# Performance work log

Measured on AMD Instinct MI355X. Metric: run time of the kernel, lower is better.

## Reference

```python
import jax, jax.numpy as jnp
import numpy as np

NEG_SLOPE = 0.2
LN_EPS = 1e-5


def _gat_layer(x, src, dst, W, a_src, a_dst, N):
    # x: [N, Fin], W: [Fin, H*C], a_src/a_dst: [H, C]
    H, C = a_src.shape
    h = (x @ W).reshape(N, H, C)
    al_src = (h * a_src).sum(-1)  # [N, H]
    al_dst = (h * a_dst).sum(-1)  # [N, H]
    e = jax.nn.leaky_relu(al_src[src] + al_dst[dst], NEG_SLOPE)  # [E, H]
    m = jax.ops.segment_max(e, dst, num_segments=N)
    e = jnp.exp(e - m[dst])
    denom = jax.ops.segment_sum(e, dst, num_segments=N)
    alpha = e / denom[dst]  # softmax over incoming edges per dst node
    msg = h[src] * alpha[:, :, None]  # [E, H, C]
    return jax.ops.segment_sum(msg, dst, num_segments=N)  # [N, H, C]


def _layer_norm(x, g, b):
    mu = x.mean(-1, keepdims=True)
    var = ((x - mu) ** 2).mean(-1, keepdims=True)
    return (x - mu) * jax.lax.rsqrt(var + LN_EPS) * g + b


def setup_inputs() -> dict:
    key = jax.random.key(0)
    ks = jax.random.split(key, 20)
    N, E, Fin, Ch, H = 50000, 800000, 128, 64, 4
    s = lambda k, shp, sc=0.05: jax.random.normal(k, shp, dtype=jnp.float32) * sc
    return {
        "x": jax.random.normal(ks[0], (N, Fin), dtype=jnp.float32),
        "edge_index": jax.random.randint(ks[1], (2, E), 0, N, dtype=jnp.int64),
        "W1": s(ks[2], (Fin, H * Ch)),
        "att_src1": s(ks[3], (H, Ch)),
        "att_dst1": s(ks[4], (H, Ch)),
        "b1": jnp.zeros((H * Ch,), jnp.float32),
        "ln1_g": jnp.ones((H * Ch,), jnp.float32),
        "ln1_b": jnp.zeros((H * Ch,), jnp.float32),
        "W2": s(ks[5], (H * Ch, Ch)),
        "att_src2": s(ks[6], (1, Ch)),
        "att_dst2": s(ks[7], (1, Ch)),
        "b2": jnp.zeros((Ch,), jnp.float32),
        "ln2_g": jnp.ones((Ch,), jnp.float32),
        "ln2_b": jnp.zeros((Ch,), jnp.float32),
        "fc1_W": s(ks[8], (Ch, Ch // 2)),
        "fc1_b": jnp.zeros((Ch // 2,), jnp.float32),
        "fc2_W": s(ks[9], (Ch // 2, 1)),
        "fc2_b": jnp.zeros((1,), jnp.float32),
    }


def reference(x, edge_index, W1, att_src1, att_dst1, b1, ln1_g, ln1_b,
              W2, att_src2, att_dst2, b2, ln2_g, ln2_b,
              fc1_W, fc1_b, fc2_W, fc2_b):
    N = x.shape[0]
    # PyG GATConv adds self-loops by default
    loop = jnp.arange(N, dtype=edge_index.dtype)
    src = jnp.concatenate([edge_index[0], loop])
    dst = jnp.concatenate([edge_index[1], loop])

    # GAT layer 1 (heads=4, concat) + LayerNorm + ReLU (dropout is identity in eval)
    h = _gat_layer(x, src, dst, W1, att_src1, att_dst1, N).reshape(N, -1) + b1
    h = jax.nn.relu(_layer_norm(h, ln1_g, ln1_b))

    # GAT layer 2 (heads=1) + LayerNorm + ReLU
    h = _gat_layer(h, src, dst, W2, att_src2, att_dst2, N).reshape(N, -1) + b2
    h = jax.nn.relu(_layer_norm(h, ln2_g, ln2_b))

    # MLP head
    h = jax.nn.relu(h @ fc1_W + fc1_b)
    return h @ fc2_W + fc2_b  # [N, 1]
```

## Files before the change

### kernel.cpp

```cpp
#include <hip/hip_runtime.h>
#include <hip/hip_fp16.h>
#include <math.h>

#define NEG_SLOPE 0.2f
#define LN_EPS 1e-5f
#define SCCHUNK 8192
#define PADCAP 64
#define CURPAD 32

typedef __attribute__((ext_vector_type(8))) _Float16 half8;
typedef __attribute__((ext_vector_type(4))) _Float16 half4;
typedef __attribute__((ext_vector_type(4))) float floatx4;

static __device__ __forceinline__ float lrelu(float e) {
    return e > 0.0f ? e : NEG_SLOPE * e;
}

__global__ __launch_bounds__(256) void k_scatter(
    const int* __restrict__ ei, unsigned* __restrict__ cursor,
    unsigned short* __restrict__ eidx, int N, int E)
{
    const int tid = threadIdx.x;
    const unsigned basev = cursor[(size_t)N * CURPAD];
    const int Et = E + N;
    const int i0 = blockIdx.x * SCCHUNK;

    int s[32], d[32];
    unsigned pos[32];

#pragma unroll
    for (int j = 0; j < 32; ++j) {
        const int i = i0 + j * 256 + tid;
        if (i < Et) {
            if (i < E) { s[j] = ei[i]; d[j] = ei[E + i]; }
            else       { s[j] = d[j] = i - E; }
        } else {
            d[j] = -1;
        }
    }
#pragma unroll
    for (int j = 0; j < 32; ++j) {
        if (d[j] >= 0)
            pos[j] = atomicAdd(&cursor[(size_t)d[j] * CURPAD], 1u);
    }
#pragma unroll
    for (int j = 0; j < 32; ++j) {
        if (d[j] >= 0) {
            unsigned p = pos[j] - basev;
            if (p < PADCAP) eidx[(size_t)d[j] * PADCAP + p] = (unsigned short)s[j];
        }
    }
}

__global__ __launch_bounds__(256) void k_gemm1(
    const float* __restrict__ x, const float* __restrict__ W1,
    const float* __restrict__ as1, const float* __restrict__ ad1,
    _Float16* __restrict__ h1, float* __restrict__ als, float* __restrict__ ald,
    int N)
{
    const int tid = threadIdx.x;
    const int lane = tid & 63, w = tid >> 6;
    const int l15 = lane & 15, quad = lane >> 4;
    const int r_base = blockIdx.x * 64;

    half8 B[4][4];
    float asv[4], adv[4];
#pragma unroll
    for (int nt = 0; nt < 4; ++nt) {
        const int n = w * 64 + nt * 16 + l15;
        asv[nt] = as1[n]; adv[nt] = ad1[n];
#pragma unroll
        for (int ks = 0; ks < 4; ++ks) {
            const int k0 = ks * 32 + quad * 8;
            half8 b;
#pragma unroll
            for (int j = 0; j < 8; ++j) b[j] = (_Float16)W1[(size_t)(k0 + j) * 256 + n];
            B[ks][nt] = b;
        }
    }

#pragma unroll
    for (int rt = 0; rt < 4; ++rt) {
        const int r0 = r_base + rt * 16;
        int m = r0 + l15; if (m >= N) m = N - 1;
        half8 A[4];
#pragma unroll
        for (int ks = 0; ks < 4; ++ks) {
            const int k0 = ks * 32 + quad * 8;
            const float4* xp = (const float4*)(x + (size_t)m * 128 + k0);
            float4 v0 = xp[0], v1 = xp[1];
            half8 a;
            a[0] = (_Float16)v0.x; a[1] = (_Float16)v0.y; a[2] = (_Float16)v0.z; a[3] = (_Float16)v0.w;
            a[4] = (_Float16)v1.x; a[5] = (_Float16)v1.y; a[6] = (_Float16)v1.z; a[7] = (_Float16)v1.w;
            A[ks] = a;
        }
        floatx4 C[4];
#pragma unroll
        for (int nt = 0; nt < 4; ++nt) C[nt] = (floatx4){0.f, 0.f, 0.f, 0.f};
#pragma unroll
        for (int ks = 0; ks < 4; ++ks)
#pragma unroll
            for (int nt = 0; nt < 4; ++nt)
                C[nt] = __builtin_amdgcn_mfma_f32_16x16x32_f16(A[ks], B[ks][nt], C[nt], 0, 0, 0);

#pragma unroll
        for (int reg = 0; reg < 4; ++reg) {
            const int row = r0 + quad * 4 + reg;
            float vs = 0.f, vd = 0.f;
#pragma unroll
            for (int nt = 0; nt < 4; ++nt) {
                float c = C[nt][reg];
                if (row < N) h1[(size_t)row * 256 + w * 64 + nt * 16 + l15] = (_Float16)c;
                vs += c * asv[nt]; vd += c * adv[nt];
            }
#pragma unroll
            for (int o = 1; o < 16; o <<= 1) { vs += __shfl_xor(vs, o); vd += __shfl_xor(vd, o); }
            if (l15 == 0 && row < N) { als[row * 4 + w] = vs; ald[row * 4 + w] = vd; }
        }
    }
}

__global__ __launch_bounds__(256) void k_agg1(
    const _Float16* __restrict__ h1, const float* __restrict__ als, const float* __restrict__ ald,
    const unsigned* __restrict__ cursor, const unsigned short* __restrict__ eidx,
    const float* __restrict__ b1, const float* __restrict__ g1, const float* __restrict__ be1,
    _Float16* __restrict__ hln1, int N)
{
    __shared__ float alp[4][64][4];
    const int wv = threadIdx.x >> 6, lane = threadIdx.x & 63;
    int n = blockIdx.x * 4 + wv;
    if (n >= N) n = N - 1;
    const int base = n * PADCAP;
    const unsigned basev = cursor[(size_t)N * CURPAD];
    int deg = (int)(cursor[(size_t)n * CURPAD] - basev); if (deg > PADCAP) deg = PADCAP;
    const float4 ad = ((const float4*)ald)[n];

    const int srcv = eidx[base + (lane < deg ? lane : deg - 1)];
    float e0 = -1e30f, e1 = -1e30f, e2 = -1e30f, e3 = -1e30f;
    if (lane < deg) {
        float4 a4 = ((const float4*)als)[srcv];
        e0 = lrelu(a4.x + ad.x);
        e1 = lrelu(a4.y + ad.y);
        e2 = lrelu(a4.z + ad.z);
        e3 = lrelu(a4.w + ad.w);
    }
    float m0 = e0, m1 = e1, m2 = e2, m3 = e3;
#pragma unroll
    for (int o = 32; o; o >>= 1) {
        m0 = fmaxf(m0, __shfl_xor(m0, o));
        m1 = fmaxf(m1, __shfl_xor(m1, o));
        m2 = fmaxf(m2, __shfl_xor(m2, o));
        m3 = fmaxf(m3, __shfl_xor(m3, o));
    }
    float p0 = __expf(e0 - m0), p1 = __expf(e1 - m1);
    float p2 = __expf(e2 - m2), p3 = __expf(e3 - m3);
    float s0 = p0, s1 = p1, s2 = p2, s3 = p3;
#pragma unroll
    for (int o = 32; o; o >>= 1) {
        s0 += __shfl_xor(s0, o);
        s1 += __shfl_xor(s1, o);
        s2 += __shfl_xor(s2, o);
        s3 += __shfl_xor(s3, o);
    }
    float4 av;
    av.x = p0 / s0; av.y = p1 / s1; av.z = p2 / s2; av.w = p3 / s3;
    *(float4*)(&alp[wv][lane][0]) = av;

    float4 acc = make_float4(0.f, 0.f, 0.f, 0.f);
    const int hd = lane >> 4;
    const float* alpr = &alp[wv][0][hd];
    const int degr = (deg + 7) & ~7;
    for (int eb = 0; eb < degr; eb += 8) {
#pragma unroll
        for (int u = 0; u < 8; ++u) {
            const int e = eb + u;
            int s = __builtin_amdgcn_readlane(srcv, e);
            float a_e = alpr[e * 4];
            half4 v = *(const half4*)(h1 + (size_t)s * 256 + 4 * lane);
            acc.x = fmaf((float)v.x, a_e, acc.x);
            acc.y = fmaf((float)v.y, a_e, acc.y);
            acc.z = fmaf((float)v.z, a_e, acc.z);
            acc.w = fmaf((float)v.w, a_e, acc.w);
        }
    }

    float4 bb = ((const float4*)b1)[lane];
    float y0 = acc.x + bb.x, y1 = acc.y + bb.y, y2 = acc.z + bb.z, y3 = acc.w + bb.w;
    float ps = y0 + y1 + y2 + y3;
    float pss = y0 * y0 + y1 * y1 + y2 * y2 + y3 * y3;
#pragma unroll
    for (int o = 32; o; o >>= 1) { ps += __shfl_xor(ps, o); pss += __shfl_xor(pss, o); }
    float mu = ps * (1.f / 256.f);
    float var = pss * (1.f / 256.f) - mu * mu;
    float rstd = rsqrtf(var + LN_EPS);
    float4 gg = ((const float4*)g1)[lane];
    float4 b2v = ((const float4*)be1)[lane];
    half4 outv;
    outv.x = (_Float16)fmaxf((y0 - mu) * rstd * gg.x + b2v.x, 0.f);
    outv.y = (_Float16)fmaxf((y1 - mu) * rstd * gg.y + b2v.y, 0.f);
    outv.z = (_Float16)fmaxf((y2 - mu) * rstd * gg.z + b2v.z, 0.f);
    outv.w = (_Float16)fmaxf((y3 - mu) * rstd * gg.w + b2v.w, 0.f);
    ((half4*)(hln1 + (size_t)n * 256))[lane] = outv;
}

__global__ __launch_bounds__(256) void k_gemm2(
    const _Float16* __restrict__ hln1, const float* __restrict__ W2,
    const float* __restrict__ as2, const float* __restrict__ ad2,
    _Float16* __restrict__ h2, float* __restrict__ als2, float* __restrict__ ald2, int N)
{
    __shared__ float ps_s[4][64], ps_d[4][64];
    const int lane = threadIdx.x & 63, w = threadIdx.x >> 6;
    const int l15 = lane & 15, quad = lane >> 4;
    const int r_base = blockIdx.x * 64;

    const int n = w * 16 + l15;
    const float asv = as2[n], adv = ad2[n];
    half8 B[8];
#pragma unroll
    for (int ks = 0; ks < 8; ++ks) {
        const int k0 = ks * 32 + quad * 8;
        half8 b;
#pragma unroll
        for (int j = 0; j < 8; ++j) b[j] = (_Float16)W2[(size_t)(k0 + j) * 64 + n];
        B[ks] = b;
    }

#pragma unroll
    for (int rt = 0; rt < 4; ++rt) {
        const int r0 = r_base + rt * 16;
        int m = r0 + l15; if (m >= N) m = N - 1;
        floatx4 C = (floatx4){0.f, 0.f, 0.f, 0.f};
#pragma unroll
        for (int ks = 0; ks < 8; ++ks) {
            half8 a = *(const half8*)(hln1 + (size_t)m * 256 + ks * 32 + quad * 8);
            C = __builtin_amdgcn_mfma_f32_16x16x32_f16(a, B[ks], C, 0, 0, 0);
        }
#pragma unroll
        for (int reg = 0; reg < 4; ++reg) {
            const int row = r0 + quad * 4 + reg;
            float c = C[reg];
            if (row < N) h2[(size_t)row * 64 + n] = (_Float16)c;
            float vs = c * asv, vd = c * adv;
#pragma unroll
            for (int o = 1; o < 16; o <<= 1) { vs += __shfl_xor(vs, o); vd += __shfl_xor(vd, o); }
            if (l15 == 0) {
                ps_s[w][rt * 16 + quad * 4 + reg] = vs;
                ps_d[w][rt * 16 + quad * 4 + reg] = vd;
            }
        }
    }
    __syncthreads();
    const int t = threadIdx.x;
    if (t < 64) {
        const int row = r_base + t;
        if (row < N) {
            als2[row] = ps_s[0][t] + ps_s[1][t] + ps_s[2][t] + ps_s[3][t];
            ald2[row] = ps_d[0][t] + ps_d[1][t] + ps_d[2][t] + ps_d[3][t];
        }
    }
}

__global__ __launch_bounds__(256) void k_agg2(
    const _Float16* __restrict__ h2, const float* __restrict__ als, const float* __restrict__ ald,
    const unsigned* __restrict__ cursor, const unsigned short* __restrict__ eidx,
    const float* __restrict__ b2, const float* __restrict__ g2, const float* __restrict__ be2,
    const float* __restrict__ fc1W, const float* __restrict__ fc1b,
    const float* __restrict__ fc2W, const float* __restrict__ fc2b,
    float* __restrict__ out, int N)
{
    __shared__ float sh[4][64];
    const int wv = threadIdx.x >> 6, lane = threadIdx.x & 63;
    int n = blockIdx.x * 4 + wv;
    if (n >= N) n = N - 1;
    const int base = n * PADCAP;
    const unsigned basev = cursor[(size_t)N * CURPAD];
    int deg = (int)(cursor[(size_t)n * CURPAD] - basev); if (deg > PADCAP) deg = PADCAP;
    const float adn = ald[n];

    const int srcv = eidx[base + (lane < deg ? lane : deg - 1)];
    float e = -1e30f;
    if (lane < deg) e = lrelu(als[srcv] + adn);
    float m = e;
#pragma unroll
    for (int o = 32; o; o >>= 1) m = fmaxf(m, __shfl_xor(m, o));
    float p = __expf(e - m);
    float s = p;
#pragma unroll
    for (int o = 32; o; o >>= 1) s += __shfl_xor(s, o);
    const float alpha = p / s;

    float acc = 0.f;
    const int degr = (deg + 7) & ~7;
    for (int eb = 0; eb < degr; eb += 8) {
#pragma unroll
        for (int u = 0; u < 8; ++u) {
            const int e2 = eb + u;
            int sidx = __builtin_amdgcn_readlane(srcv, e2);
            float a_e = __int_as_float(
                __builtin_amdgcn_readlane(__float_as_int(alpha), e2));
            acc = fmaf((float)h2[(size_t)sidx * 64 + lane], a_e, acc);
        }
    }

    float y = acc + b2[lane];
    float ps = y, pss = y * y;
#pragma unroll
    for (int o = 32; o; o >>= 1) { ps += __shfl_xor(ps, o); pss += __shfl_xor(pss, o); }
    float mu = ps * (1.f / 64.f);
    float var = pss * (1.f / 64.f) - mu * mu;
    float r = fmaxf((y - mu) * rsqrtf(var + LN_EPS) * g2[lane] + be2[lane], 0.f);

    sh[wv][lane] = r;

    if (lane < 32) {
        float a1 = fc1b[lane];
#pragma unroll 8
        for (int k = 0; k < 64; ++k) a1 += sh[wv][k] * fc1W[k * 32 + lane];
        a1 = fmaxf(a1, 0.f);
        float t = a1 * fc2W[lane];
#pragma unroll
        for (int o = 16; o; o >>= 1) t += __shfl_xor(t, o);
        if (lane == 0) out[n] = t + fc2b[0];
    }
}

extern "C" void kernel_launch(void* const* d_in, const int* in_sizes, int n_in,
                              void* d_out, int out_size, void* d_ws, size_t ws_size,
                              hipStream_t stream)
{
    const float* x   = (const float*)d_in[0];
    const int* ei    = (const int*)d_in[1];
    const float* W1  = (const float*)d_in[2];
    const float* as1 = (const float*)d_in[3];
    const float* ad1 = (const float*)d_in[4];
    const float* b1  = (const float*)d_in[5];
    const float* g1  = (const float*)d_in[6];
    const float* be1 = (const float*)d_in[7];
    const float* W2  = (const float*)d_in[8];
    const float* as2 = (const float*)d_in[9];
    const float* ad2 = (const float*)d_in[10];
    const float* b2  = (const float*)d_in[11];
    const float* g2  = (const float*)d_in[12];
    const float* be2 = (const float*)d_in[13];
    const float* fc1W = (const float*)d_in[14];
    const float* fc1b = (const float*)d_in[15];
    const float* fc2W = (const float*)d_in[16];
    const float* fc2b = (const float*)d_in[17];
    float* out = (float*)d_out;

    const int N = in_sizes[0] / 128;
    const int E = in_sizes[1] / 2;
    const int Et = E + N;
    const int nsc = (Et + SCCHUNK - 1) / SCCHUNK;
    const int ntiles = (N + 63) / 64;

    char* p = (char*)d_ws;
    auto carve = [&](size_t bytes) {
        void* q = p;
        p += (bytes + 255) & ~(size_t)255;
        return q;
    };
    _Float16* h1    = (_Float16*)carve((size_t)N * 256 * 2);
    _Float16* hln1h = (_Float16*)carve((size_t)N * 256 * 2);
    _Float16* h2    = (_Float16*)carve((size_t)N * 64 * 2);
    float* als1 = (float*)carve((size_t)N * 4 * 4);
    float* ald1 = (float*)carve((size_t)N * 4 * 4);
    float* als2 = (float*)carve((size_t)N * 4);
    float* ald2 = (float*)carve((size_t)N * 4);
    unsigned* cursor = (unsigned*)carve((size_t)(N + 1) * CURPAD * 4);
    unsigned short* eidx = (unsigned short*)carve((size_t)N * PADCAP * 2);

    k_scatter<<<nsc, 256, 0, stream>>>(ei, cursor, eidx, N, E);
    k_gemm1<<<ntiles, 256, 0, stream>>>(x, W1, as1, ad1, h1, als1, ald1, N);
    k_agg1<<<(N + 3) / 4, 256, 0, stream>>>(h1, als1, ald1, cursor, eidx, b1, g1, be1, hln1h, N);
    k_gemm2<<<(N + 63) / 64, 256, 0, stream>>>(hln1h, W2, as2, ad2, h2, als2, ald2, N);
    k_agg2<<<(N + 3) / 4, 256, 0, stream>>>(h2, als2, ald2, cursor, eidx,
                                            b2, g2, be2, fc1W, fc1b, fc2W, fc2b, out, N);
}
```

Measured before the change: 307.1 us.

## Fuse scatter into gemm1 launch and fuse agg1 with gemm2 via LDS

Merges the edge scatter kernel into the first GEMM launch as extra blocks, so both run concurrently in one grid. Fuses layer-1 aggregation/LayerNorm with the layer-2 GEMM: 16 nodes per 1024-thread block write their normalized features to shared memory, and 4 waves do the MFMA on them. This removes the hln1 global round-trip and two launches. In exchange, W2 is reloaded from global per block, 12 of 16 waves idle during the GEMM, and 1024-thread blocks may reduce occupancy.

```diff
diff --git a/kernel.cpp b/kernel.cpp
--- a/kernel.cpp
+++ b/kernel.cpp
@@ -16,52 +16,52 @@
     return e > 0.0f ? e : NEG_SLOPE * e;
 }
 
-__global__ __launch_bounds__(256) void k_scatter(
-    const int* __restrict__ ei, unsigned* __restrict__ cursor,
-    unsigned short* __restrict__ eidx, int N, int E)
-{
-    const int tid = threadIdx.x;
-    const unsigned basev = cursor[(size_t)N * CURPAD];
-    const int Et = E + N;
-    const int i0 = blockIdx.x * SCCHUNK;
-
-    int s[32], d[32];
-    unsigned pos[32];
-
-#pragma unroll
-    for (int j = 0; j < 32; ++j) {
-        const int i = i0 + j * 256 + tid;
-        if (i < Et) {
-            if (i < E) { s[j] = ei[i]; d[j] = ei[E + i]; }
-            else       { s[j] = d[j] = i - E; }
-        } else {
-            d[j] = -1;
-        }
-    }
-#pragma unroll
-    for (int j = 0; j < 32; ++j) {
-        if (d[j] >= 0)
-            pos[j] = atomicAdd(&cursor[(size_t)d[j] * CURPAD], 1u);
-    }
-#pragma unroll
-    for (int j = 0; j < 32; ++j) {
-        if (d[j] >= 0) {
-            unsigned p = pos[j] - basev;
-            if (p < PADCAP) eidx[(size_t)d[j] * PADCAP + p] = (unsigned short)s[j];
-        }
-    }
-}
-
-__global__ __launch_bounds__(256) void k_gemm1(
+__global__ __launch_bounds__(256) void k_g1sc(
     const float* __restrict__ x, const float* __restrict__ W1,
     const float* __restrict__ as1, const float* __restrict__ ad1,
     _Float16* __restrict__ h1, float* __restrict__ als, float* __restrict__ ald,
-    int N)
+    const int* __restrict__ ei, unsigned* __restrict__ cursor,
+    unsigned short* __restrict__ eidx,
+    int N, int E, int nsc)
 {
     const int tid = threadIdx.x;
+
+    if ((int)blockIdx.x < nsc) {
+        const unsigned basev = cursor[(size_t)N * CURPAD];
+        const int Et = E + N;
+        const int i0 = blockIdx.x * SCCHUNK;
+
+        int s[32], d[32];
+        unsigned pos[32];
+#pragma unroll
+        for (int j = 0; j < 32; ++j) {
+            const int i = i0 + j * 256 + tid;
+            if (i < Et) {
+                if (i < E) { s[j] = ei[i]; d[j] = ei[E + i]; }
+                else       { s[j] = d[j] = i - E; }
+            } else {
+                d[j] = -1;
+            }
+        }
+#pragma unroll
+        for (int j = 0; j < 32; ++j) {
+            if (d[j] >= 0)
+                pos[j] = atomicAdd(&cursor[(size_t)d[j] * CURPAD], 1u);
+        }
+#pragma unroll
+        for (int j = 0; j < 32; ++j) {
+            if (d[j] >= 0) {
+                unsigned p = pos[j] - basev;
+                if (p < PADCAP) eidx[(size_t)d[j] * PADCAP + p] = (unsigned short)s[j];
+            }
+        }
+        return;
+    }
+
+    const int tile = blockIdx.x - nsc;
     const int lane = tid & 63, w = tid >> 6;
     const int l15 = lane & 15, quad = lane >> 4;
-    const int r_base = blockIdx.x * 64;
+    const int r_base = tile * 64;
 
     half8 B[4][4];
     float asv[4], adv[4];
@@ -120,15 +120,20 @@
     }
 }
 
-__global__ __launch_bounds__(256) void k_agg1(
+__global__ __launch_bounds__(1024) void k_agg1g2(
     const _Float16* __restrict__ h1, const float* __restrict__ als, const float* __restrict__ ald,
     const unsigned* __restrict__ cursor, const unsigned short* __restrict__ eidx,
     const float* __restrict__ b1, const float* __restrict__ g1, const float* __restrict__ be1,
-    _Float16* __restrict__ hln1, int N)
+    const float* __restrict__ W2, const float* __restrict__ as2, const float* __restrict__ ad2,
+    _Float16* __restrict__ h2, float* __restrict__ als2, float* __restrict__ ald2, int N)
 {
-    __shared__ float alp[4][64][4];
+    __shared__ float alp[16][64][4];
+    __shared__ _Float16 hln[16][264];
+    __shared__ float ps_s[4][16], ps_d[4][16];
+
     const int wv = threadIdx.x >> 6, lane = threadIdx.x & 63;
-    int n = blockIdx.x * 4 + wv;
+    const int nb = blockIdx.x * 16;
+    int n = nb + wv;
     if (n >= N) n = N - 1;
     const int base = n * PADCAP;
     const unsigned basev = cursor[(size_t)N * CURPAD];
@@ -200,63 +205,43 @@
     outv.y = (_Float16)fmaxf((y1 - mu) * rstd * gg.y + b2v.y, 0.f);
     outv.z = (_Float16)fmaxf((y2 - mu) * rstd * gg.z + b2v.z, 0.f);
     outv.w = (_Float16)fmaxf((y3 - mu) * rstd * gg.w + b2v.w, 0.f);
-    ((half4*)(hln1 + (size_t)n * 256))[lane] = outv;
-}
-
-__global__ __launch_bounds__(256) void k_gemm2(
-    const _Float16* __restrict__ hln1, const float* __restrict__ W2,
-    const float* __restrict__ as2, const float* __restrict__ ad2,
-    _Float16* __restrict__ h2, float* __restrict__ als2, float* __restrict__ ald2, int N)
-{
-    __shared__ float ps_s[4][64], ps_d[4][64];
-    const int lane = threadIdx.x & 63, w = threadIdx.x >> 6;
+    *(half4*)(&hln[wv][lane * 4]) = outv;
+
+    __syncthreads();
+
     const int l15 = lane & 15, quad = lane >> 4;
-    const int r_base = blockIdx.x * 64;
-
-    const int n = w * 16 + l15;
-    const float asv = as2[n], adv = ad2[n];
-    half8 B[8];
-#pragma unroll
-    for (int ks = 0; ks < 8; ++ks) {
-        const int k0 = ks * 32 + quad * 8;
-        half8 b;
-#pragma unroll
-        for (int j = 0; j < 8; ++j) b[j] = (_Float16)W2[(size_t)(k0 + j) * 64 + n];
-        B[ks] = b;
-    }
-
-#pragma unroll
-    for (int rt = 0; rt < 4; ++rt) {
-        const int r0 = r_base + rt * 16;
-        int m = r0 + l15; if (m >= N) m = N - 1;
+    if (wv < 4) {
+        const int ct = wv;
+        const int nch = ct * 16 + l15;
+        const float asv = as2[nch], adv = ad2[nch];
         floatx4 C = (floatx4){0.f, 0.f, 0.f, 0.f};
 #pragma unroll
         for (int ks = 0; ks < 8; ++ks) {
-            half8 a = *(const half8*)(hln1 + (size_t)m * 256 + ks * 32 + quad * 8);
-            C = __builtin_amdgcn_mfma_f32_16x16x32_f16(a, B[ks], C, 0, 0, 0);
+            const int k0 = ks * 32 + quad * 8;
+            half8 a = *(const half8*)(&hln[l15][k0]);
+            half8 b;
+#pragma unroll
+            for (int j = 0; j < 8; ++j) b[j] = (_Float16)W2[(size_t)(k0 + j) * 64 + nch];
+            C = __builtin_amdgcn_mfma_f32_16x16x32_f16(a, b, C, 0, 0, 0);
         }
 #pragma unroll
         for (int reg = 0; reg < 4; ++reg) {
-            const int row = r0 + quad * 4 + reg;
+            const int m = quad * 4 + reg;
+            int row = nb + m; if (row >= N) row = N - 1;
             float c = C[reg];
-            if (row < N) h2[(size_t)row * 64 + n] = (_Float16)c;
+            h2[(size_t)row * 64 + nch] = (_Float16)c;
             float vs = c * asv, vd = c * adv;
 #pragma unroll
             for (int o = 1; o < 16; o <<= 1) { vs += __shfl_xor(vs, o); vd += __shfl_xor(vd, o); }
-            if (l15 == 0) {
-                ps_s[w][rt * 16 + quad * 4 + reg] = vs;
-                ps_d[w][rt * 16 + quad * 4 + reg] = vd;
-            }
+            if (l15 == 0) { ps_s[ct][m] = vs; ps_d[ct][m] = vd; }
         }
     }
     __syncthreads();
     const int t = threadIdx.x;
-    if (t < 64) {
-        const int row = r_base + t;
-        if (row < N) {
-            als2[row] = ps_s[0][t] + ps_s[1][t] + ps_s[2][t] + ps_s[3][t];
-            ald2[row] = ps_d[0][t] + ps_d[1][t] + ps_d[2][t] + ps_d[3][t];
-        }
+    if (t < 16) {
+        int row = nb + t; if (row >= N) row = N - 1;
+        als2[row] = ps_s[0][t] + ps_s[1][t] + ps_s[2][t] + ps_s[3][t];
+        ald2[row] = ps_d[0][t] + ps_d[1][t] + ps_d[2][t] + ps_d[3][t];
     }
 }
 
@@ -361,7 +346,6 @@
         return q;
     };
     _Float16* h1    = (_Float16*)carve((size_t)N * 256 * 2);
-    _Float16* hln1h = (_Float16*)carve((size_t)N * 256 * 2);
     _Float16* h2    = (_Float16*)carve((size_t)N * 64 * 2);
     float* als1 = (float*)carve((size_t)N * 4 * 4);
     float* ald1 = (float*)carve((size_t)N * 4 * 4);
@@ -370,10 +354,11 @@
     unsigned* cursor = (unsigned*)carve((size_t)(N + 1) * CURPAD * 4);
     unsigned short* eidx = (unsigned short*)carve((size_t)N * PADCAP * 2);
 
-    k_scatter<<<nsc, 256, 0, stream>>>(ei, cursor, eidx, N, E);
-    k_gemm1<<<ntiles, 256, 0, stream>>>(x, W1, as1, ad1, h1, als1, ald1, N);
-    k_agg1<<<(N + 3) / 4, 256, 0, stream>>>(h1, als1, ald1, cursor, eidx, b1, g1, be1, hln1h, N);
-    k_gemm2<<<(N + 63) / 64, 256, 0, stream>>>(hln1h, W2, as2, ad2, h2, als2, ald2, N);
+    k_g1sc<<<nsc + ntiles, 256, 0, stream>>>(x, W1, as1, ad1, h1, als1, ald1,
+                                             ei, cursor, eidx, N, E, nsc);
+    k_agg1g2<<<(N + 15) / 16, 1024, 0, stream>>>(h1, als1, ald1, cursor, eidx,
+                                                 b1, g1, be1, W2, as2, ad2,
+                                                 h2, als2, ald2, N);
     k_agg2<<<(N + 3) / 4, 256, 0, stream>>>(h2, als2, ald2, cursor, eidx,
                                             b2, g2, be2, fc1W, fc1b, fc2W, fc2b, out, N);
 }
```

New measurement: 282.2 us. 1.09x faster.
